# Optimization experiments

Hardware: AMD Instinct MI355X
Metric: run time of the kernel (lower is better)

The kernel has to match this reference:

```python
import jax, jax.numpy as jnp
import numpy as np

B, L, H, ED, NCONV = 64, 2048, 128, 4, 3
N = B * L


def gat(x, src, dst, edge_attr, W, a_s, a_d, We, a_e, b, self_loops):
    """PyG GATConv, heads=1, concat=True, negative_slope=0.2, fill_value='mean'."""
    n = x.shape[0]
    h = x @ W                              # [N,H]
    a_src = h @ a_s                        # [N]
    a_dst = h @ a_d                        # [N]
    alpha = a_src[src] + a_dst[dst] + (edge_attr @ We) @ a_e  # [E]
    if self_loops:
        ones = jnp.ones(src.shape[0], x.dtype)
        deg = jax.ops.segment_sum(ones, dst, num_segments=n)
        mean_attr = jax.ops.segment_sum(edge_attr, dst, num_segments=n) / jnp.maximum(deg, 1.0)[:, None]
        loop_alpha = a_src + a_dst + (mean_attr @ We) @ a_e
        idx = jnp.arange(n, dtype=src.dtype)
        src = jnp.concatenate([src, idx])
        dst = jnp.concatenate([dst, idx])
        alpha = jnp.concatenate([alpha, loop_alpha])
    alpha = jax.nn.leaky_relu(alpha, 0.2)
    m = jax.ops.segment_max(alpha, dst, num_segments=n)
    ex = jnp.exp(alpha - m[dst])
    den = jax.ops.segment_sum(ex, dst, num_segments=n)
    coef = ex / jnp.maximum(den, 1e-16)[dst]
    return jax.ops.segment_sum(coef[:, None] * h[src], dst, num_segments=n) + b


def setup_inputs() -> dict:
    key = jax.random.key(0)
    ks = iter(jax.random.split(key, 32))
    # binary trees: per graph, node k>0 has parent (k-1)//2; edge child->parent (to_up)
    local = np.arange(1, L)
    parent = (local - 1) // 2
    offs = (np.arange(B) * L)[:, None]
    src = jnp.asarray((local[None, :] + offs).ravel(), dtype=jnp.int32)
    dst = jnp.asarray((parent[None, :] + offs).ravel(), dtype=jnp.int32)
    E = src.shape[0]
    s = 0.1
    inp = {
        "x": jax.random.normal(next(ks), (N,), jnp.float32),
        "src": src,
        "dst": dst,
        "edge_attr": jax.random.normal(next(ks), (E, ED), jnp.float32),
        "up_W0": jax.random.normal(next(ks), (1, H)) * s,
        "up_W": jax.random.normal(next(ks), (NCONV - 1, H, H)) * s,
        "up_att_src": jax.random.normal(next(ks), (NCONV, H)) * s,
        "up_att_dst": jax.random.normal(next(ks), (NCONV, H)) * s,
        "up_We": jax.random.normal(next(ks), (NCONV, ED, H)) * s,
        "up_att_edge": jax.random.normal(next(ks), (NCONV, H)) * s,
        "up_b": jax.random.normal(next(ks), (NCONV, H)) * s,
        "down_W": jax.random.normal(next(ks), (NCONV - 1, H, H)) * s,
        "down_att_src": jax.random.normal(next(ks), (NCONV - 1, H)) * s,
        "down_att_dst": jax.random.normal(next(ks), (NCONV - 1, H)) * s,
        "down_We": jax.random.normal(next(ks), (NCONV - 1, ED, H)) * s,
        "down_att_edge": jax.random.normal(next(ks), (NCONV - 1, H)) * s,
        "down_b": jax.random.normal(next(ks), (NCONV - 1, H)) * s,
        "lin_W": jax.random.normal(next(ks), (NCONV - 1, H, H)) * s,
        "lin_b": jax.random.normal(next(ks), (NCONV - 1, H)) * s,
        "lin_last_W": jax.random.normal(next(ks), (H, 1)) * s,
        "lin_last_b": jax.random.normal(next(ks), (1,)) * s,
    }
    return inp


def reference(x, src, dst, edge_attr, up_W0, up_W, up_att_src, up_att_dst, up_We,
              up_att_edge, up_b, down_W, down_att_src, down_att_dst, down_We,
              down_att_edge, down_b, lin_W, lin_b, lin_last_W, lin_last_b):
    h = x[:, None]                                            # flat_c.view(-1,1)
    # upward pass: toup GATConvs (with self loops) + relu
    for i in range(NCONV):
        W = up_W0 if i == 0 else up_W[i - 1]
        h = jax.nn.relu(gat(h, src, dst, edge_attr, W, up_att_src[i], up_att_dst[i],
                            up_We[i], up_att_edge[i], up_b[i], True))
    x_up = h
    # downward pass uses reversed edges, no self loops; replicates original's
    # indexing bug (todown[0] used twice, todown[-1] never used)
    src_d, dst_d = dst, src
    x_down = jax.nn.relu(gat(x_up, src_d, dst_d, edge_attr, down_W[0], down_att_src[0],
                             down_att_dst[0], down_We[0], down_att_edge[0], down_b[0], False))
    xx = x_down + x_up
    for i in range(NCONV - 1):
        xx = jax.nn.relu(xx @ lin_W[i] + lin_b[i])
        x_down = jax.nn.relu(gat(xx, src_d, dst_d, edge_attr, down_W[i], down_att_src[i],
                                 down_att_dst[i], down_We[i], down_att_edge[i], down_b[i], False))
        xx = x_down + x_up
    final_emb = xx
    out_nodes = xx @ lin_last_W + lin_last_b                  # [N,1]
    batch_out = out_nodes.reshape(B, L)                       # all graphs are max_len
    batch_emb = final_emb.reshape(B, L, H)
    out = batch_out - batch_out[:, :1]                        # subtract root node
    return out, batch_emb
```

## Files before the change

kernel.cpp:

```cpp
#include <hip/hip_runtime.h>
#include <hip/hip_bf16.h>
#include <cstdint>
#include <cstddef>

typedef unsigned short u16;
typedef short bf16x8 __attribute__((ext_vector_type(8)));
typedef float f32x4 __attribute__((ext_vector_type(4)));

#define Bn 64
#define Ln 2048
#define Hn 128
#define EDn 4
#define Nn (Bn*Ln)

#define CV_W0    0
#define CV_WUP   128
#define CV_AS    32896
#define CV_AD    33280
#define CV_WE    33664
#define CV_AE    35200
#define CV_BUP   35584
#define CV_WD    35968
#define CV_BD    68736
#define CV_WL    68992
#define CV_BL    101760
#define CV_WLAST 102016
#define CV_TOTAL 102144

__device__ __forceinline__ float b2f(u16 u) {
  union { float f; unsigned int i; } v; v.i = ((unsigned int)u) << 16; return v.f;
}
__device__ __forceinline__ u16 f2b(float f) {
  __hip_bfloat16 h = __float2bfloat16(f);
  union { __hip_bfloat16 h; u16 u; } v; v.h = h; return v.u;
}
__device__ __forceinline__ float lrelu(float v) { return v >= 0.f ? v : 0.2f * v; }
__device__ __forceinline__ float wave_sum(float r) {
  #pragma unroll
  for (int off = 32; off > 0; off >>= 1) r += __shfl_xor(r, off, 64);
  return r;
}
__device__ __forceinline__ float ld_in(const void* p, size_t i, int f) {
  return f ? b2f(((const u16*)p)[i]) : ((const float*)p)[i];
}
__device__ __forceinline__ u16* Cbase(void* dout, int f) {
  return f ? ((u16*)dout + Nn) : (u16*)((float*)dout + Nn);
}
__device__ __forceinline__ float lo16(unsigned v) { return b2f((u16)(v & 0xFFFF)); }
__device__ __forceinline__ float hi16(unsigned v) { return b2f((u16)(v >> 16)); }

__global__ void detect_kernel(const u16* __restrict__ x, int* __restrict__ flag) {
  int lane = threadIdx.x;
  u16 u = x[lane];
  int e = (u >> 7) & 0xFF;
  bool good = (e >= 100 && e <= 140) || ((u & 0x7FFF) == 0);
  unsigned long long m = __ballot(good);
  if (lane == 0) *flag = (__popcll(m) >= 56) ? 1 : 0;
}

struct CvtArgs { const void* src[12]; int off[12]; int tr[12]; };
__global__ void cvt_kernel(CvtArgs a, const int* __restrict__ flagp, u16* __restrict__ dst) {
  int f = *flagp;
  int i = blockIdx.x * 256 + threadIdx.x;
  if (i >= CV_TOTAL) return;
  int s = 0;
  #pragma unroll
  for (int k = 1; k < 12; ++k) s = (i >= a.off[k]) ? k : s;
  int j = i - a.off[s];
  int sj = j;
  if (a.tr[s]) {
    int mat = j >> 14, rr = (j >> 7) & 127, cc = j & 127;
    sj = (mat << 14) + cc * 128 + rr;
  }
  dst[i] = f ? ((const u16*)a.src[s])[sj] : f2b(((const float*)a.src[s])[sj]);
}

__global__ void up0_kernel(const void* __restrict__ x, const void* __restrict__ edge_attr,
                           const u16* __restrict__ W0, const u16* __restrict__ att_s,
                           const u16* __restrict__ att_d, const u16* __restrict__ We0,
                           const u16* __restrict__ ae0, const u16* __restrict__ b0,
                           u16* __restrict__ y, const int* __restrict__ flagp) {
  __shared__ float P[6];
  __shared__ float comb[64];
  __shared__ float W0s[Hn];
  __shared__ float b0s[Hn];
  int f = *flagp;
  int t = threadIdx.x;
  int lane = t & 63, w = t >> 6;
  if (w < 2) {
    const u16* vb = (w == 0) ? att_s : att_d;
    float r = b2f(W0[lane]) * b2f(vb[lane]) + b2f(W0[lane+64]) * b2f(vb[lane+64]);
    r = wave_sum(r);
    if (lane == 0) P[w] = r;
  } else {
    int e0 = (w - 2) * 2;
    float a0 = b2f(ae0[lane]), a1 = b2f(ae0[lane+64]);
    float r0 = b2f(We0[e0*Hn+lane])*a0     + b2f(We0[e0*Hn+lane+64])*a1;
    float r1 = b2f(We0[(e0+1)*Hn+lane])*a0 + b2f(We0[(e0+1)*Hn+lane+64])*a1;
    r0 = wave_sum(r0); r1 = wave_sum(r1);
    if (lane == 0) { P[2+e0] = r0; P[3+e0] = r1; }
  }
  if (t < Hn) { W0s[t] = b2f(W0[t]); b0s[t] = b2f(b0[t]); }
  __syncthreads();
  int base = blockIdx.x * 64;
  if (t < 64) {
    int n = base + t;
    int local = n & (Ln - 1);
    int nb = n >> 11;
    int root = n - local;
    float S0 = P[0], D0 = P[1];
    float w0 = P[2], w1 = P[3], w2 = P[4], w3 = P[5];
    float xp = ld_in(x, n, f);
    float ad_p = D0 * xp;
    int c1l = 2*local + 1, c2l = 2*local + 2;
    int deg = (c1l < Ln ? 1 : 0) + (c2l < Ln ? 1 : 0);
    float e1 = 0.f, e2 = 0.f, xc1 = 0.f, xc2 = 0.f, sc1 = 0.f, sc2 = 0.f;
    if (deg >= 1) {
      xc1 = ld_in(x, root + c1l, f);
      size_t ei = ((size_t)nb*(Ln-1) + (c1l-1))*EDn;
      e1 = ld_in(edge_attr, ei+0, f)*w0 + ld_in(edge_attr, ei+1, f)*w1
         + ld_in(edge_attr, ei+2, f)*w2 + ld_in(edge_attr, ei+3, f)*w3;
      sc1 = lrelu(S0*xc1 + ad_p + e1);
    }
    if (deg == 2) {
      xc2 = ld_in(x, root + c2l, f);
      size_t ei = ((size_t)nb*(Ln-1) + (c2l-1))*EDn;
      e2 = ld_in(edge_attr, ei+0, f)*w0 + ld_in(edge_attr, ei+1, f)*w1
         + ld_in(edge_attr, ei+2, f)*w2 + ld_in(edge_attr, ei+3, f)*w3;
      sc2 = lrelu(S0*xc2 + ad_p + e2);
    }
    float mean_e = deg ? (e1 + e2) / (float)deg : 0.f;
    float ss = lrelu(S0*xp + ad_p + mean_e);
    float m = ss;
    if (deg >= 1) m = fmaxf(m, sc1);
    if (deg == 2) m = fmaxf(m, sc2);
    float es  = __expf(ss - m);
    float ec1 = (deg >= 1) ? __expf(sc1 - m) : 0.f;
    float ec2 = (deg == 2) ? __expf(sc2 - m) : 0.f;
    float den = es + ec1 + ec2;
    comb[t] = (es*xp + ec1*xc1 + ec2*xc2) / den;
  }
  __syncthreads();
  u16* out = y + (size_t)base * Hn;
  for (int i = t; i < 64*Hn/4; i += 256) {
    int row = i >> 5;
    int col = (i & 31) * 4;
    float c = comb[row];
    ushort4 st;
    st.x = f2b(fmaxf(c*W0s[col+0] + b0s[col+0], 0.f));
    st.y = f2b(fmaxf(c*W0s[col+1] + b0s[col+1], 0.f));
    st.z = f2b(fmaxf(c*W0s[col+2] + b0s[col+2], 0.f));
    st.w = f2b(fmaxf(c*W0s[col+3] + b0s[col+3], 0.f));
    *(ushort4*)&out[(size_t)i*4] = st;
  }
}

template<int GATHER, int EPI, int ASAD>
__global__ __launch_bounds__(256, 2) void gemm_k(
                       const u16* __restrict__ Xp, const u16* __restrict__ Wt,
                       const u16* __restrict__ bias, const u16* __restrict__ Uarr,
                       u16* __restrict__ outp, void* __restrict__ dout,
                       const int* __restrict__ flagp, int x_is_C, int out_mode,
                       float2* __restrict__ asad, const u16* __restrict__ avs,
                       const u16* __restrict__ avd, float* __restrict__ nodesp) {
  __shared__ u16 Ws[Hn*Hn];
  int f = *flagp;
  const u16* X = x_is_C ? Cbase(dout, f) : Xp;
  int t = threadIdx.x;
  int lane = t & 63, w = t >> 6;
  int m = lane & 15, q = lane >> 4;
  #pragma unroll
  for (int i = 0; i < 8; ++i) {
    int g = t + 256*i; int r = g >> 4, u = g & 15;
    uint4 v = ((const uint4*)Wt)[g];
    *(uint4*)&Ws[(r*16 + (u ^ (r & 15)))*8] = v;
  }
  int row0 = blockIdx.x * 256;
  int wbase = row0 + w*64;
  uint4 xf[4][4];
  #pragma unroll
  for (int rt = 0; rt < 4; ++rt) {
    int R = wbase + rt*16 + m;
    bool zero = false;
    const uint4* src;
    if (GATHER) {
      int local = R & (Ln - 1);
      if (local == 0) { zero = true; src = (const uint4*)X; }
      else src = (const uint4*)(X + (size_t)((R - local) + ((local - 1) >> 1))*Hn);
    } else {
      src = (const uint4*)(X + (size_t)R*Hn);
    }
    #pragma unroll
    for (int ki = 0; ki < 4; ++ki) {
      uint4 v = src[ki*4 + q];
      if (zero) { v.x = 0; v.y = 0; v.z = 0; v.w = 0; }
      xf[rt][ki] = v;
    }
  }
  __syncthreads();
  f32x4 acc[4][8];
  #pragma unroll
  for (int rt = 0; rt < 4; ++rt)
    #pragma unroll
    for (int ct = 0; ct < 8; ++ct) acc[rt][ct] = (f32x4){0.f, 0.f, 0.f, 0.f};
  #pragma unroll
  for (int ki = 0; ki < 4; ++ki) {
    #pragma unroll
    for (int ct = 0; ct < 8; ++ct) {
      bf16x8 wf = *(bf16x8*)&Ws[((ct*16 + m)*16 + ((ki*4 + q) ^ m))*8];
      #pragma unroll
      for (int rt = 0; rt < 4; ++rt)
        acc[rt][ct] = __builtin_amdgcn_mfma_f32_16x16x32_bf16(
                        wf, *(bf16x8*)&xf[rt][ki], acc[rt][ct], 0, 0, 0);
    }
  }
  u16* Cb = Cbase(dout, f);
  float* emf = (float*)dout + Nn;
  u16* od = (out_mode == 0) ? outp : (out_mode == 1 ? Cb : (u16*)dout + Nn);
  #pragma unroll
  for (int rt = 0; rt < 4; ++rt) {
    int R = wbase + rt*16 + m;
    float asv = 0.f, adv = 0.f;
    #pragma unroll
    for (int ct = 0; ct < 8; ++ct) {
      int c0 = ct*16 + q*4;
      float o[4];
      #pragma unroll
      for (int r = 0; r < 4; ++r) o[r] = acc[rt][ct][r];
      if (ASAD == 1) {
        ushort4 sv = *(const ushort4*)&avs[c0];
        ushort4 dv = *(const ushort4*)&avd[c0];
        asv += o[0]*b2f(sv.x) + o[1]*b2f(sv.y) + o[2]*b2f(sv.z) + o[3]*b2f(sv.w);
        adv += o[0]*b2f(dv.x) + o[1]*b2f(dv.y) + o[2]*b2f(dv.z) + o[3]*b2f(dv.w);
      }
      if (EPI >= 1) {
        ushort4 bv = *(const ushort4*)&bias[c0];
        o[0] = fmaxf(o[0] + b2f(bv.x), 0.f); o[1] = fmaxf(o[1] + b2f(bv.y), 0.f);
        o[2] = fmaxf(o[2] + b2f(bv.z), 0.f); o[3] = fmaxf(o[3] + b2f(bv.w), 0.f);
      }
      if (EPI == 2) {
        ushort4 uv = *(const ushort4*)&Uarr[(size_t)R*Hn + c0];
        o[0] += b2f(uv.x); o[1] += b2f(uv.y); o[2] += b2f(uv.z); o[3] += b2f(uv.w);
      }
      if (ASAD == 2) {
        ushort4 sv = *(const ushort4*)&avs[c0];
        asv += o[0]*b2f(sv.x) + o[1]*b2f(sv.y) + o[2]*b2f(sv.z) + o[3]*b2f(sv.w);
      }
      if (out_mode == 2 && !f) {
        float4 fv; fv.x = o[0]; fv.y = o[1]; fv.z = o[2]; fv.w = o[3];
        *(float4*)&emf[(size_t)R*Hn + c0] = fv;
      } else {
        ushort4 st; st.x = f2b(o[0]); st.y = f2b(o[1]); st.z = f2b(o[2]); st.w = f2b(o[3]);
        *(ushort4*)&od[(size_t)R*Hn + c0] = st;
      }
    }
    if (ASAD == 1) {
      asv += __shfl_xor(asv, 16, 64); asv += __shfl_xor(asv, 32, 64);
      adv += __shfl_xor(adv, 16, 64); adv += __shfl_xor(adv, 32, 64);
      if (q == 0) { float2 v; v.x = asv; v.y = adv; asad[R] = v; }
    }
    if (ASAD == 2) {
      asv += __shfl_xor(asv, 16, 64); asv += __shfl_xor(asv, 32, 64);
      if (q == 0) nodesp[R] = asv;
    }
  }
}

__global__ void coef_kernel(const void* __restrict__ edge_attr,
                            const u16* __restrict__ We, const u16* __restrict__ ae,
                            const float2* __restrict__ asad, float2* __restrict__ coef,
                            const int* __restrict__ flagp) {
  __shared__ float P[4];
  int f = *flagp;
  int t = threadIdx.x;
  int lane = t & 63, w = t >> 6;
  {
    unsigned av = *(const unsigned*)&ae[2*lane];
    unsigned wv = *(const unsigned*)&We[w*Hn + 2*lane];
    float r = wave_sum(lo16(wv)*lo16(av) + hi16(wv)*hi16(av));
    if (lane == 0) P[w] = r;
  }
  __syncthreads();
  int p = blockIdx.x * 256 + t;
  int local = p & (Ln - 1);
  int root = p - local;
  int nb = p >> 11;
  int c1l = 2*local + 1, c2l = 2*local + 2;
  int deg = (c1l < Ln ? 1 : 0) + (c2l < Ln ? 1 : 0);
  float2 aa = asad[p];
  float w0 = P[0], w1 = P[1], w2 = P[2], w3 = P[3];
  float e1 = 0.f, e2 = 0.f, sc1 = 0.f, sc2 = 0.f;
  if (deg >= 1) {
    size_t ei = ((size_t)nb*(Ln-1) + (c1l-1))*EDn;
    if (f) {
      ushort4 v = *(const ushort4*)((const u16*)edge_attr + ei);
      e1 = b2f(v.x)*w0 + b2f(v.y)*w1 + b2f(v.z)*w2 + b2f(v.w)*w3;
      if (deg == 2) {
        ushort4 v2 = *(const ushort4*)((const u16*)edge_attr + ei + EDn);
        e2 = b2f(v2.x)*w0 + b2f(v2.y)*w1 + b2f(v2.z)*w2 + b2f(v2.w)*w3;
      }
    } else {
      float4 v = *(const float4*)((const float*)edge_attr + ei);
      e1 = v.x*w0 + v.y*w1 + v.z*w2 + v.w*w3;
      if (deg == 2) {
        float4 v2 = *(const float4*)((const float*)edge_attr + ei + EDn);
        e2 = v2.x*w0 + v2.y*w1 + v2.z*w2 + v2.w*w3;
      }
    }
    sc1 = lrelu(asad[root + c1l].x + aa.y + e1);
    if (deg == 2) sc2 = lrelu(asad[root + c2l].x + aa.y + e2);
  }
  float mean_e = deg ? (e1 + e2) / (float)deg : 0.f;
  float ss = lrelu(aa.x + aa.y + mean_e);
  float m = ss;
  if (deg >= 1) m = fmaxf(m, sc1);
  if (deg == 2) m = fmaxf(m, sc2);
  float es  = __expf(ss - m);
  float ec1 = (deg >= 1) ? __expf(sc1 - m) : 0.f;
  float ec2 = (deg == 2) ? __expf(sc2 - m) : 0.f;
  float inv = 1.f / (es + ec1 + ec2);
  float2 cf; cf.x = ec1 * inv; cf.y = ec2 * inv;
  coef[p] = cf;
}

__global__ void blend_kernel(const float2* __restrict__ coef, const u16* __restrict__ bias,
                             u16* __restrict__ y, void* __restrict__ dout,
                             const int* __restrict__ flagp) {
  int f = *flagp;
  const u16* h = Cbase(dout, f);
  int t = threadIdx.x;
  int g = t & 15;
  int p = blockIdx.x * 16 + (t >> 4);
  int local = p & (Ln - 1);
  int root = p - local;
  int c1l = 2*local + 1, c2l = 2*local + 2;
  int deg = (c1l < Ln ? 1 : 0) + (c2l < Ln ? 1 : 0);
  float2 cf = coef[p];
  float es = 1.f - cf.x - cf.y;
  int off = g * 8;
  uint4 hp = *(const uint4*)&h[(size_t)p*Hn + off];
  uint4 h1 = {0,0,0,0}, h2 = {0,0,0,0};
  if (deg >= 1) h1 = *(const uint4*)&h[(size_t)(root + c1l)*Hn + off];
  if (deg == 2) h2 = *(const uint4*)&h[(size_t)(root + c2l)*Hn + off];
  uint4 bv = *(const uint4*)&bias[off];
  uint4 st;
  #pragma unroll
  for (int i = 0; i < 4; ++i) {
    unsigned a = ((unsigned*)&hp)[i], b1 = ((unsigned*)&h1)[i];
    unsigned b2 = ((unsigned*)&h2)[i], bb = ((unsigned*)&bv)[i];
    float o0 = es*lo16(a) + cf.x*lo16(b1) + cf.y*lo16(b2) + lo16(bb);
    float o1 = es*hi16(a) + cf.x*hi16(b1) + cf.y*hi16(b2) + hi16(bb);
    ((unsigned*)&st)[i] = (unsigned)f2b(fmaxf(o0, 0.f)) | ((unsigned)f2b(fmaxf(o1, 0.f)) << 16);
  }
  *(uint4*)&y[(size_t)p*Hn + off] = st;
}

__global__ void score_kernel(const float* __restrict__ nodes, void* __restrict__ dout,
                             const int* __restrict__ flagp) {
  int f = *flagp;
  int n = blockIdx.x * 256 + threadIdx.x;
  float v = nodes[n] - nodes[n & ~(Ln - 1)];
  if (f) ((u16*)dout)[n] = f2b(v);
  else   ((float*)dout)[n] = v;
}

extern "C" void kernel_launch(void* const* d_in, const int* in_sizes, int n_in,
                              void* d_out, int out_size, void* d_ws, size_t ws_size,
                              hipStream_t stream) {
  const void* x         = d_in[0];
  const void* edge_attr = d_in[3];

  u16* Ubuf = (u16*)d_ws;
  u16* Abuf = Ubuf + (size_t)Nn*Hn;
  u16* cvt  = Abuf + (size_t)Nn*Hn;
  float2* asad = (float2*)(cvt + CV_TOTAL);
  float2* coef = asad + Nn;
  float* nodes = (float*)(coef + Nn);
  int* flag = (int*)(nodes + Nn);

  detect_kernel<<<1, 64, 0, stream>>>((const u16*)d_in[0], flag);

  CvtArgs ca;
  ca.src[0]  = d_in[4];  ca.off[0]  = CV_W0;    ca.tr[0]  = 0;
  ca.src[1]  = d_in[5];  ca.off[1]  = CV_WUP;   ca.tr[1]  = 1;
  ca.src[2]  = d_in[6];  ca.off[2]  = CV_AS;    ca.tr[2]  = 0;
  ca.src[3]  = d_in[7];  ca.off[3]  = CV_AD;    ca.tr[3]  = 0;
  ca.src[4]  = d_in[8];  ca.off[4]  = CV_WE;    ca.tr[4]  = 0;
  ca.src[5]  = d_in[9];  ca.off[5]  = CV_AE;    ca.tr[5]  = 0;
  ca.src[6]  = d_in[10]; ca.off[6]  = CV_BUP;   ca.tr[6]  = 0;
  ca.src[7]  = d_in[11]; ca.off[7]  = CV_WD;    ca.tr[7]  = 1;
  ca.src[8]  = d_in[16]; ca.off[8]  = CV_BD;    ca.tr[8]  = 0;
  ca.src[9]  = d_in[17]; ca.off[9]  = CV_WL;    ca.tr[9]  = 1;
  ca.src[10] = d_in[18]; ca.off[10] = CV_BL;    ca.tr[10] = 0;
  ca.src[11] = d_in[19]; ca.off[11] = CV_WLAST; ca.tr[11] = 0;
  cvt_kernel<<<(CV_TOTAL + 255)/256, 256, 0, stream>>>(ca, flag, cvt);

  up0_kernel<<<Nn/64, 256, 0, stream>>>(x, edge_attr, cvt+CV_W0, cvt+CV_AS, cvt+CV_AD,
                                        cvt+CV_WE, cvt+CV_AE, cvt+CV_BUP, Abuf, flag);
  gemm_k<0,0,1><<<Nn/256, 256, 0, stream>>>(Abuf, cvt+CV_WUP, nullptr, nullptr,
                                         nullptr, d_out, flag, 0, 1,
                                         asad, cvt+CV_AS+Hn, cvt+CV_AD+Hn, nullptr);
  coef_kernel<<<Nn/256, 256, 0, stream>>>(edge_attr, cvt+CV_WE+EDn*Hn, cvt+CV_AE+Hn,
                                          asad, coef, flag);
  blend_kernel<<<Nn/16, 256, 0, stream>>>(coef, cvt+CV_BUP+Hn, Abuf, d_out, flag);
  gemm_k<0,0,1><<<Nn/256, 256, 0, stream>>>(Abuf, cvt+CV_WUP+Hn*Hn, nullptr, nullptr,
                                         nullptr, d_out, flag, 0, 1,
                                         asad, cvt+CV_AS+2*Hn, cvt+CV_AD+2*Hn, nullptr);
  coef_kernel<<<Nn/256, 256, 0, stream>>>(edge_attr, cvt+CV_WE+2*EDn*Hn, cvt+CV_AE+2*Hn,
                                          asad, coef, flag);
  blend_kernel<<<Nn/16, 256, 0, stream>>>(coef, cvt+CV_BUP+2*Hn, Ubuf, d_out, flag);

  gemm_k<1,2,0><<<Nn/256, 256, 0, stream>>>(Ubuf, cvt+CV_WD, cvt+CV_BD, Ubuf,
                                         nullptr, d_out, flag, 0, 1,
                                         nullptr, nullptr, nullptr, nullptr);
  gemm_k<0,1,0><<<Nn/256, 256, 0, stream>>>(nullptr, cvt+CV_WL, cvt+CV_BL, nullptr,
                                         Abuf, d_out, flag, 1, 0,
                                         nullptr, nullptr, nullptr, nullptr);
  gemm_k<1,2,0><<<Nn/256, 256, 0, stream>>>(Abuf, cvt+CV_WD, cvt+CV_BD, Ubuf,
                                         nullptr, d_out, flag, 0, 1,
                                         nullptr, nullptr, nullptr, nullptr);
  gemm_k<0,1,0><<<Nn/256, 256, 0, stream>>>(nullptr, cvt+CV_WL+Hn*Hn, cvt+CV_BL+Hn, nullptr,
                                         Abuf, d_out, flag, 1, 0,
                                         nullptr, nullptr, nullptr, nullptr);
  gemm_k<1,2,2><<<Nn/256, 256, 0, stream>>>(Abuf, cvt+CV_WD+Hn*Hn, cvt+CV_BD+Hn, Ubuf,
                                         nullptr, d_out, flag, 0, 2,
                                         nullptr, cvt+CV_WLAST, nullptr, nodes);

  score_kernel<<<Nn/256, 256, 0, stream>>>(nodes, d_out, flag);
}
```

Baseline: 294.1 us.

## Fuse blend into next GEMM and chain down-GAT with linear layer in one kernel

Folds the first attention blend into the following up-GEMM, so blended features are computed straight into registers instead of making a round trip through memory. Each downward GAT GEMM is fused with the next linear layer, keeping the intermediate tile in shared memory, which removes kernel launches and full N×H intermediate traffic. It also issues the per-row activation loads before the weight-tile staging in gemm_k to overlap latency. In exchange it adds a third workspace buffer, a 64KB shared-memory footprint in the fused kernel that may lower occupancy, and it reads the blend neighbours redundantly.

Result: faster. 267.7 us (-9.0%).

```diff
diff --git a/kernel.cpp b/kernel.cpp
--- a/kernel.cpp
+++ b/kernel.cpp
@@ -169,12 +169,6 @@
   int t = threadIdx.x;
   int lane = t & 63, w = t >> 6;
   int m = lane & 15, q = lane >> 4;
-  #pragma unroll
-  for (int i = 0; i < 8; ++i) {
-    int g = t + 256*i; int r = g >> 4, u = g & 15;
-    uint4 v = ((const uint4*)Wt)[g];
-    *(uint4*)&Ws[(r*16 + (u ^ (r & 15)))*8] = v;
-  }
   int row0 = blockIdx.x * 256;
   int wbase = row0 + w*64;
   uint4 xf[4][4];
@@ -197,6 +191,12 @@
       xf[rt][ki] = v;
     }
   }
+  #pragma unroll
+  for (int i = 0; i < 8; ++i) {
+    int g = t + 256*i; int r = g >> 4, u = g & 15;
+    uint4 v = ((const uint4*)Wt)[g];
+    *(uint4*)&Ws[(r*16 + (u ^ (r & 15)))*8] = v;
+  }
   __syncthreads();
   f32x4 acc[4][8];
   #pragma unroll
@@ -262,6 +262,210 @@
     if (ASAD == 2) {
       asv += __shfl_xor(asv, 16, 64); asv += __shfl_xor(asv, 32, 64);
       if (q == 0) nodesp[R] = asv;
+    }
+  }
+}
+
+__global__ __launch_bounds__(256, 2) void gemm_blend_k(
+                       const u16* __restrict__ Wt, const float2* __restrict__ coef,
+                       const u16* __restrict__ bias_up, u16* __restrict__ outp,
+                       void* __restrict__ dout, const int* __restrict__ flagp,
+                       float2* __restrict__ asad, const u16* __restrict__ avs,
+                       const u16* __restrict__ avd) {
+  __shared__ u16 Ws[Hn*Hn];
+  int f = *flagp;
+  const u16* h = Cbase(dout, f);
+  int t = threadIdx.x;
+  int lane = t & 63, w = t >> 6;
+  int m = lane & 15, q = lane >> 4;
+  int row0 = blockIdx.x * 256;
+  int wbase = row0 + w*64;
+  uint4 xf[4][4];
+  #pragma unroll
+  for (int rt = 0; rt < 4; ++rt) {
+    int R = wbase + rt*16 + m;
+    int local = R & (Ln - 1);
+    int root = R - local;
+    int c1l = 2*local + 1, c2l = 2*local + 2;
+    int r1 = (c1l < Ln) ? root + c1l : R;
+    int r2 = (c2l < Ln) ? root + c2l : R;
+    float2 cf = coef[R];
+    float es = 1.f - cf.x - cf.y;
+    const uint4* hp = (const uint4*)(h + (size_t)R*Hn);
+    const uint4* h1 = (const uint4*)(h + (size_t)r1*Hn);
+    const uint4* h2 = (const uint4*)(h + (size_t)r2*Hn);
+    #pragma unroll
+    for (int ki = 0; ki < 4; ++ki) {
+      int u = ki*4 + q;
+      uint4 a = hp[u], b = h1[u], c = h2[u];
+      uint4 bv = ((const uint4*)bias_up)[u];
+      uint4 st;
+      #pragma unroll
+      for (int i = 0; i < 4; ++i) {
+        unsigned av = ((unsigned*)&a)[i], b1v = ((unsigned*)&b)[i];
+        unsigned b2v = ((unsigned*)&c)[i], bbv = ((unsigned*)&bv)[i];
+        float o0 = es*lo16(av) + cf.x*lo16(b1v) + cf.y*lo16(b2v) + lo16(bbv);
+        float o1 = es*hi16(av) + cf.x*hi16(b1v) + cf.y*hi16(b2v) + hi16(bbv);
+        ((unsigned*)&st)[i] = (unsigned)f2b(fmaxf(o0, 0.f))
+                            | ((unsigned)f2b(fmaxf(o1, 0.f)) << 16);
+      }
+      xf[rt][ki] = st;
+    }
+  }
+  #pragma unroll
+  for (int i = 0; i < 8; ++i) {
+    int g = t + 256*i; int r = g >> 4, u = g & 15;
+    uint4 v = ((const uint4*)Wt)[g];
+    *(uint4*)&Ws[(r*16 + (u ^ (r & 15)))*8] = v;
+  }
+  __syncthreads();
+  f32x4 acc[4][8];
+  #pragma unroll
+  for (int rt = 0; rt < 4; ++rt)
+    #pragma unroll
+    for (int ct = 0; ct < 8; ++ct) acc[rt][ct] = (f32x4){0.f, 0.f, 0.f, 0.f};
+  #pragma unroll
+  for (int ki = 0; ki < 4; ++ki) {
+    #pragma unroll
+    for (int ct = 0; ct < 8; ++ct) {
+      bf16x8 wf = *(bf16x8*)&Ws[((ct*16 + m)*16 + ((ki*4 + q) ^ m))*8];
+      #pragma unroll
+      for (int rt = 0; rt < 4; ++rt)
+        acc[rt][ct] = __builtin_amdgcn_mfma_f32_16x16x32_bf16(
+                        wf, *(bf16x8*)&xf[rt][ki], acc[rt][ct], 0, 0, 0);
+    }
+  }
+  #pragma unroll
+  for (int rt = 0; rt < 4; ++rt) {
+    int R = wbase + rt*16 + m;
+    float asv = 0.f, adv = 0.f;
+    #pragma unroll
+    for (int ct = 0; ct < 8; ++ct) {
+      int c0 = ct*16 + q*4;
+      float o0 = acc[rt][ct][0], o1 = acc[rt][ct][1];
+      float o2 = acc[rt][ct][2], o3 = acc[rt][ct][3];
+      ushort4 sv = *(const ushort4*)&avs[c0];
+      ushort4 dv = *(const ushort4*)&avd[c0];
+      asv += o0*b2f(sv.x) + o1*b2f(sv.y) + o2*b2f(sv.z) + o3*b2f(sv.w);
+      adv += o0*b2f(dv.x) + o1*b2f(dv.y) + o2*b2f(dv.z) + o3*b2f(dv.w);
+      ushort4 st; st.x = f2b(o0); st.y = f2b(o1); st.z = f2b(o2); st.w = f2b(o3);
+      *(ushort4*)&outp[(size_t)R*Hn + c0] = st;
+    }
+    asv += __shfl_xor(asv, 16, 64); asv += __shfl_xor(asv, 32, 64);
+    adv += __shfl_xor(adv, 16, 64); adv += __shfl_xor(adv, 32, 64);
+    if (q == 0) { float2 v; v.x = asv; v.y = adv; asad[R] = v; }
+  }
+}
+
+__global__ __launch_bounds__(256, 2) void fused_down_lin_k(
+                       const u16* __restrict__ Xp, const u16* __restrict__ Wdt,
+                       const u16* __restrict__ bd, const u16* __restrict__ Uarr,
+                       const u16* __restrict__ Wlt, const u16* __restrict__ bl,
+                       u16* __restrict__ outp) {
+  __shared__ u16 Ws[Hn*Hn];
+  __shared__ u16 XX[128*Hn];
+  int t = threadIdx.x;
+  int lane = t & 63, w = t >> 6;
+  int m = lane & 15, q = lane >> 4;
+  int row0 = blockIdx.x * 128;
+  int wbase = row0 + w*32;
+  uint4 xf[2][4];
+  #pragma unroll
+  for (int rt = 0; rt < 2; ++rt) {
+    int R = wbase + rt*16 + m;
+    int local = R & (Ln - 1);
+    bool zero = (local == 0);
+    const uint4* src = zero ? (const uint4*)Xp
+                     : (const uint4*)(Xp + (size_t)((R - local) + ((local - 1) >> 1))*Hn);
+    #pragma unroll
+    for (int ki = 0; ki < 4; ++ki) {
+      uint4 v = src[ki*4 + q];
+      if (zero) { v.x = 0; v.y = 0; v.z = 0; v.w = 0; }
+      xf[rt][ki] = v;
+    }
+  }
+  #pragma unroll
+  for (int i = 0; i < 8; ++i) {
+    int g = t + 256*i; int r = g >> 4, u = g & 15;
+    uint4 v = ((const uint4*)Wdt)[g];
+    *(uint4*)&Ws[(r*16 + (u ^ (r & 15)))*8] = v;
+  }
+  __syncthreads();
+  f32x4 acc[2][8];
+  #pragma unroll
+  for (int rt = 0; rt < 2; ++rt)
+    #pragma unroll
+    for (int ct = 0; ct < 8; ++ct) acc[rt][ct] = (f32x4){0.f, 0.f, 0.f, 0.f};
+  #pragma unroll
+  for (int ki = 0; ki < 4; ++ki) {
+    #pragma unroll
+    for (int ct = 0; ct < 8; ++ct) {
+      bf16x8 wf = *(bf16x8*)&Ws[((ct*16 + m)*16 + ((ki*4 + q) ^ m))*8];
+      #pragma unroll
+      for (int rt = 0; rt < 2; ++rt)
+        acc[rt][ct] = __builtin_amdgcn_mfma_f32_16x16x32_bf16(
+                        wf, *(bf16x8*)&xf[rt][ki], acc[rt][ct], 0, 0, 0);
+    }
+  }
+  __syncthreads();
+  #pragma unroll
+  for (int rt = 0; rt < 2; ++rt) {
+    int R = wbase + rt*16 + m;
+    int rl = w*32 + rt*16 + m;
+    #pragma unroll
+    for (int ct = 0; ct < 8; ++ct) {
+      int c0 = ct*16 + q*4;
+      ushort4 bv = *(const ushort4*)&bd[c0];
+      ushort4 uv = *(const ushort4*)&Uarr[(size_t)R*Hn + c0];
+      float o0 = fmaxf(acc[rt][ct][0] + b2f(bv.x), 0.f) + b2f(uv.x);
+      float o1 = fmaxf(acc[rt][ct][1] + b2f(bv.y), 0.f) + b2f(uv.y);
+      float o2 = fmaxf(acc[rt][ct][2] + b2f(bv.z), 0.f) + b2f(uv.z);
+      float o3 = fmaxf(acc[rt][ct][3] + b2f(bv.w), 0.f) + b2f(uv.w);
+      int uu = (2*ct + (q >> 1)) ^ m;
+      uint2 pk;
+      pk.x = (unsigned)f2b(o0) | ((unsigned)f2b(o1) << 16);
+      pk.y = (unsigned)f2b(o2) | ((unsigned)f2b(o3) << 16);
+      *(uint2*)&XX[rl*Hn + uu*8 + (q & 1)*4] = pk;
+    }
+  }
+  #pragma unroll
+  for (int i = 0; i < 8; ++i) {
+    int g = t + 256*i; int r = g >> 4, u = g & 15;
+    uint4 v = ((const uint4*)Wlt)[g];
+    *(uint4*)&Ws[(r*16 + (u ^ (r & 15)))*8] = v;
+  }
+  __syncthreads();
+  f32x4 acc2[2][8];
+  #pragma unroll
+  for (int rt = 0; rt < 2; ++rt)
+    #pragma unroll
+    for (int ct = 0; ct < 8; ++ct) acc2[rt][ct] = (f32x4){0.f, 0.f, 0.f, 0.f};
+  #pragma unroll
+  for (int ki = 0; ki < 4; ++ki) {
+    #pragma unroll
+    for (int ct = 0; ct < 8; ++ct) {
+      bf16x8 wf = *(bf16x8*)&Ws[((ct*16 + m)*16 + ((ki*4 + q) ^ m))*8];
+      #pragma unroll
+      for (int rt = 0; rt < 2; ++rt) {
+        int rl = w*32 + rt*16 + m;
+        bf16x8 xb = *(bf16x8*)&XX[rl*Hn + (((ki*4 + q) ^ m))*8];
+        acc2[rt][ct] = __builtin_amdgcn_mfma_f32_16x16x32_bf16(wf, xb, acc2[rt][ct], 0, 0, 0);
+      }
+    }
+  }
+  #pragma unroll
+  for (int rt = 0; rt < 2; ++rt) {
+    int R = wbase + rt*16 + m;
+    #pragma unroll
+    for (int ct = 0; ct < 8; ++ct) {
+      int c0 = ct*16 + q*4;
+      ushort4 bv = *(const ushort4*)&bl[c0];
+      ushort4 st;
+      st.x = f2b(fmaxf(acc2[rt][ct][0] + b2f(bv.x), 0.f));
+      st.y = f2b(fmaxf(acc2[rt][ct][1] + b2f(bv.y), 0.f));
+      st.z = f2b(fmaxf(acc2[rt][ct][2] + b2f(bv.z), 0.f));
+      st.w = f2b(fmaxf(acc2[rt][ct][3] + b2f(bv.w), 0.f));
+      *(ushort4*)&outp[(size_t)R*Hn + c0] = st;
     }
   }
 }
@@ -323,11 +527,8 @@
   coef[p] = cf;
 }
 
-__global__ void blend_kernel(const float2* __restrict__ coef, const u16* __restrict__ bias,
-                             u16* __restrict__ y, void* __restrict__ dout,
-                             const int* __restrict__ flagp) {
-  int f = *flagp;
-  const u16* h = Cbase(dout, f);
+__global__ void blend_kernel(const u16* __restrict__ h, const float2* __restrict__ coef,
+                             const u16* __restrict__ bias, u16* __restrict__ y) {
   int t = threadIdx.x;
   int g = t & 15;
   int p = blockIdx.x * 16 + (t >> 4);
@@ -372,7 +573,8 @@
 
   u16* Ubuf = (u16*)d_ws;
   u16* Abuf = Ubuf + (size_t)Nn*Hn;
-  u16* cvt  = Abuf + (size_t)Nn*Hn;
+  u16* Bbuf = Abuf + (size_t)Nn*Hn;
+  u16* cvt  = Bbuf + (size_t)Nn*Hn;
   float2* asad = (float2*)(cvt + CV_TOTAL);
   float2* coef = asad + Nn;
   float* nodes = (float*)(coef + Nn);
@@ -402,27 +604,18 @@
                                          asad, cvt+CV_AS+Hn, cvt+CV_AD+Hn, nullptr);
   coef_kernel<<<Nn/256, 256, 0, stream>>>(edge_attr, cvt+CV_WE+EDn*Hn, cvt+CV_AE+Hn,
                                           asad, coef, flag);
-  blend_kernel<<<Nn/16, 256, 0, stream>>>(coef, cvt+CV_BUP+Hn, Abuf, d_out, flag);
-  gemm_k<0,0,1><<<Nn/256, 256, 0, stream>>>(Abuf, cvt+CV_WUP+Hn*Hn, nullptr, nullptr,
-                                         nullptr, d_out, flag, 0, 1,
-                                         asad, cvt+CV_AS+2*Hn, cvt+CV_AD+2*Hn, nullptr);
+  gemm_blend_k<<<Nn/256, 256, 0, stream>>>(cvt+CV_WUP+Hn*Hn, coef, cvt+CV_BUP+Hn,
+                                           Bbuf, d_out, flag,
+                                           asad, cvt+CV_AS+2*Hn, cvt+CV_AD+2*Hn);
   coef_kernel<<<Nn/256, 256, 0, stream>>>(edge_attr, cvt+CV_WE+2*EDn*Hn, cvt+CV_AE+2*Hn,
                                           asad, coef, flag);
-  blend_kernel<<<Nn/16, 256, 0, stream>>>(coef, cvt+CV_BUP+2*Hn, Ubuf, d_out, flag);
-
-  gemm_k<1,2,0><<<Nn/256, 256, 0, stream>>>(Ubuf, cvt+CV_WD, cvt+CV_BD, Ubuf,
-                                         nullptr, d_out, flag, 0, 1,
-                                         nullptr, nullptr, nullptr, nullptr);
-  gemm_k<0,1,0><<<Nn/256, 256, 0, stream>>>(nullptr, cvt+CV_WL, cvt+CV_BL, nullptr,
-                                         Abuf, d_out, flag, 1, 0,
-                                         nullptr, nullptr, nullptr, nullptr);
-  gemm_k<1,2,0><<<Nn/256, 256, 0, stream>>>(Abuf, cvt+CV_WD, cvt+CV_BD, Ubuf,
-                                         nullptr, d_out, flag, 0, 1,
-                                         nullptr, nullptr, nullptr, nullptr);
-  gemm_k<0,1,0><<<Nn/256, 256, 0, stream>>>(nullptr, cvt+CV_WL+Hn*Hn, cvt+CV_BL+Hn, nullptr,
-                                         Abuf, d_out, flag, 1, 0,
-                                         nullptr, nullptr, nullptr, nullptr);
-  gemm_k<1,2,2><<<Nn/256, 256, 0, stream>>>(Abuf, cvt+CV_WD+Hn*Hn, cvt+CV_BD+Hn, Ubuf,
+  blend_kernel<<<Nn/16, 256, 0, stream>>>(Bbuf, coef, cvt+CV_BUP+2*Hn, Ubuf);
+
+  fused_down_lin_k<<<Nn/128, 256, 0, stream>>>(Ubuf, cvt+CV_WD, cvt+CV_BD, Ubuf,
+                                               cvt+CV_WL, cvt+CV_BL, Abuf);
+  fused_down_lin_k<<<Nn/128, 256, 0, stream>>>(Abuf, cvt+CV_WD, cvt+CV_BD, Ubuf,
+                                               cvt+CV_WL+Hn*Hn, cvt+CV_BL+Hn, Bbuf);
+  gemm_k<1,2,2><<<Nn/256, 256, 0, stream>>>(Bbuf, cvt+CV_WD+Hn*Hn, cvt+CV_BD+Hn, Ubuf,
                                          nullptr, d_out, flag, 0, 2,
                                          nullptr, cvt+CV_WLAST, nullptr, nodes);
 
```
